# Kernel tuning notes

Hardware: AMD Instinct MI355X
Metric: run time of the kernel (lower is better)

The kernel has to match this reference:

```python
import jax, jax.numpy as jnp
import numpy as np

EPS = 1e-5


def gcn_conv(x, row, col, W, b, num_nodes):
    """PyG GCNConv: out = D^-1/2 (A+I) D^-1/2 (x W) + b, edges as (row=src, col=dst)."""
    loop = jnp.arange(num_nodes, dtype=row.dtype)
    r = jnp.concatenate([row, loop])
    c = jnp.concatenate([col, loop])
    ones = jnp.ones(c.shape[0], dtype=x.dtype)
    deg = jax.ops.segment_sum(ones, c, num_segments=num_nodes)
    dinv = jnp.where(deg > 0, jax.lax.rsqrt(deg), 0.0)
    norm = dinv[r] * dinv[c]                      # [E+N]
    xw = x @ W                                    # [N, out]
    msg = xw[r] * norm[:, None]                   # [E+N, out]
    out = jax.ops.segment_sum(msg, c, num_segments=num_nodes)
    return out + b


def layer_norm(h, g, b):
    mu = jnp.mean(h, axis=-1, keepdims=True)
    var = jnp.mean(jnp.square(h - mu), axis=-1, keepdims=True)
    return (h - mu) * jax.lax.rsqrt(var + EPS) * g + b


def setup_inputs() -> dict:
    key = jax.random.key(0)
    ks = jax.random.split(key, 12)
    B, S, D, H = 64, 512, 64, 128
    E = 524288
    A1, A2 = 5, 5
    N = B * S

    def xavier(k, shape):
        fan_in, fan_out = shape[0], shape[1]
        lim = np.sqrt(6.0 / (fan_in + fan_out))
        return jax.random.uniform(k, shape, jnp.float32, -lim, lim)

    return {
        "x": jax.random.normal(ks[0], (B, S, D), jnp.float32),
        "edge_index": jax.random.randint(ks[1], (2, E), 0, N, jnp.int64),
        "W1": xavier(ks[2], (D, H)),
        "b1": jnp.zeros((H,), jnp.float32),
        "W2": xavier(ks[3], (H, H)),
        "b2": jnp.zeros((H,), jnp.float32),
        "ln_g": jnp.ones((H,), jnp.float32),
        "ln_b": jnp.zeros((H,), jnp.float32),
        "Wq1": xavier(ks[4], (H, A1)),
        "bq1": jnp.zeros((A1,), jnp.float32),
        "Wq2": xavier(ks[5], (H, A2)),
        "bq2": jnp.zeros((A2,), jnp.float32),
    }


def reference(x, edge_index, W1, b1, W2, b2, ln_g, ln_b, Wq1, bq1, Wq2, bq2):
    B, S, D = x.shape
    N = B * S
    x_flat = x.reshape(N, D)
    row, col = edge_index[0], edge_index[1]
    # two GCN layers (dropout is identity in eval), relu activation, then LayerNorm
    h = jax.nn.relu(gcn_conv(x_flat, row, col, W1, b1, N))
    h = jax.nn.relu(gcn_conv(h, row, col, W2, b2, N))
    h = layer_norm(h, ln_g, ln_b)
    h = h.reshape(B, S, -1)
    # mode='q': per-action-dimension Q heads + hidden features
    q1 = h @ Wq1 + bq1
    q2 = h @ Wq2 + bq2
    return q1, q2, h
```

## Files before the change

kernel.cpp:

```cpp
#include <hip/hip_runtime.h>

#define HDIM 128
#define SLOT 64

typedef decltype(__builtin_amdgcn_cvt_pkrtz(0.0f, 0.0f)) h2;

__device__ __forceinline__ unsigned pack_h2(float a, float b) {
    h2 v = __builtin_amdgcn_cvt_pkrtz(a, b);
    return __builtin_bit_cast(unsigned, v);
}
__device__ __forceinline__ unsigned addh2(unsigned A, unsigned B) {
    h2 r = __builtin_bit_cast(h2, A) + __builtin_bit_cast(h2, B);
    return __builtin_bit_cast(unsigned, r);
}
__device__ __forceinline__ float2 h2f(unsigned A) {
    h2 v = __builtin_bit_cast(h2, A);
    return make_float2((float)v.x, (float)v.y);
}
__device__ __forceinline__ float dot2f(unsigned a, unsigned b, float c) {
#if __has_builtin(__builtin_amdgcn_fdot2)
    return __builtin_amdgcn_fdot2(__builtin_bit_cast(h2, a),
                                  __builtin_bit_cast(h2, b), c, false);
#else
    float2 fa = h2f(a), fb = h2f(b);
    return c + fa.x * fb.x + fa.y * fb.y;
#endif
}

__global__ void prep_kernel(int* __restrict__ cnt, int* __restrict__ xs1N,
                            int* __restrict__ xs2N, int N) {
    int i = blockIdx.x * blockDim.x + threadIdx.x;
    if (i < N) cnt[i] = 0;
    if (i < 64) { xs1N[i] = 0; xs2N[i] = 0; }
}

__global__ void fill_kernel(const int* __restrict__ row, const int* __restrict__ col,
                            int* __restrict__ cnt, ushort* __restrict__ slots, int E) {
    int i = blockIdx.x * blockDim.x + threadIdx.x;
    int e0 = 2 * i;
    if (e0 + 1 < E) {
        int2 r2 = *(const int2*)(row + e0);
        int2 c2 = *(const int2*)(col + e0);
        int p0 = atomicAdd(&cnt[c2.x], 1);
        if (p0 < SLOT - 1) slots[(long)c2.x * SLOT + p0] = (ushort)r2.x;
        int p1 = atomicAdd(&cnt[c2.y], 1);
        if (p1 < SLOT - 1) slots[(long)c2.y * SLOT + p1] = (ushort)r2.y;
    } else if (e0 < E) {
        int c = col[e0];
        int p = atomicAdd(&cnt[c], 1);
        if (p < SLOT - 1) slots[(long)c * SLOT + p] = (ushort)row[e0];
    }
}

template<int K, int NPB>
__global__ void gemm_scale_kernel(const float* __restrict__ X, const float* __restrict__ W,
                                  const int* __restrict__ cnt,
                                  unsigned* __restrict__ xs, int N) {
    __shared__ float xr[NPB * K];
    int t  = threadIdx.x;
    int n0 = blockIdx.x * NPB;
    for (int i = t; i < NPB * K; i += 128)
        xr[i] = X[(long)n0 * K + i];
    __syncthreads();

    float acc[NPB];
#pragma unroll
    for (int m = 0; m < NPB; ++m) acc[m] = 0.f;

    for (int k = 0; k < K; ++k) {
        float w = W[k * HDIM + t];
#pragma unroll
        for (int m = 0; m < NPB; ++m) acc[m] += xr[m * K + k] * w;
    }

#pragma unroll
    for (int m = 0; m < NPB; ++m) {
        int n = n0 + m;
        if (n < N) {
            float v = acc[m] * rsqrtf((float)(cnt[n] + 1));
            float w = __shfl_xor(v, 1);
            if (!(t & 1))
                xs[(long)n * 64 + (t >> 1)] = pack_h2(v, w);
        }
    }
}

__global__ __launch_bounds__(512)
void gather_gemm2_kernel(const int* __restrict__ cnt, const ushort* __restrict__ slots,
                         const unsigned* __restrict__ xs1,
                         const float* __restrict__ b1, const float* __restrict__ W2,
                         unsigned* __restrict__ xs2, int N) {
    __shared__ uint2 w2p[64 * 64];
    __shared__ unsigned hs2[8][64];
    int tid = threadIdx.x;
    for (int j = tid; j < 64 * 64; j += 512) {
        int kk = j >> 6;
        int c  = j & 63;
        const float* wr0 = W2 + (2 * kk) * HDIM;
        const float* wr1 = W2 + (2 * kk + 1) * HDIM;
        uint2 u;
        u.x = pack_h2(wr0[2 * c],     wr1[2 * c]);
        u.y = pack_h2(wr0[2 * c + 1], wr1[2 * c + 1]);
        w2p[j] = u;
    }
    __syncthreads();

    int wave = tid >> 6;
    int lane = tid & 63;
    int node = blockIdx.x * 8 + wave;
    if (node >= N) return;

    int degN = cnt[node];
    int degS = degN < (SLOT - 1) ? degN : (SLOT - 1);
    float di = rsqrtf((float)(degN + 1));

    int idx = N;
    if (lane == 0)          idx = node;
    else if (lane <= degS)  idx = (int)slots[(long)node * SLOT + lane - 1];

    unsigned accA = 0, accB = 0;
    int m = degS + 1;
    for (int k = 0; k < m; k += 8) {
        int r[8];
#pragma unroll
        for (int i = 0; i < 8; ++i) r[i] = __shfl(idx, k + i);
        unsigned u[8];
#pragma unroll
        for (int i = 0; i < 8; ++i) u[i] = xs1[((long)r[i] << 6) + lane];
#pragma unroll
        for (int i = 0; i < 8; i += 2) {
            accA = addh2(accA, u[i]);
            accB = addh2(accB, u[i + 1]);
        }
    }

    float2 t2 = h2f(addh2(accA, accB));
    int d0 = 2 * lane;
    float vx = t2.x * di + b1[d0];
    float vy = t2.y * di + b1[d0 + 1];
    vx = vx > 0.f ? vx : 0.f;
    vy = vy > 0.f ? vy : 0.f;

    hs2[wave][lane] = pack_h2(vx, vy);

    float a0 = 0.f, a1 = 0.f;
#pragma unroll 4
    for (int kk = 0; kk < 64; ++kk) {
        unsigned hb = hs2[wave][kk];
        uint2 w = w2p[kk * 64 + lane];
        a0 = dot2f(hb, w.x, a0);
        a1 = dot2f(hb, w.y, a1);
    }
    xs2[((long)node << 6) + lane] = pack_h2(a0 * di, a1 * di);
}

__global__ __launch_bounds__(512)
void gather_ln_kernel(const int* __restrict__ cnt, const ushort* __restrict__ slots,
                      const unsigned* __restrict__ xs,
                      const float* __restrict__ bvec, float* __restrict__ out,
                      const float* __restrict__ lng, const float* __restrict__ lnb,
                      const float* __restrict__ Wq1, const float* __restrict__ bq1,
                      const float* __restrict__ Wq2, const float* __restrict__ bq2,
                      float* __restrict__ q1, float* __restrict__ q2, int N) {
    __shared__ float w1s[HDIM * 5];
    __shared__ float w2s[HDIM * 5];
    for (int i = threadIdx.x; i < HDIM * 5; i += 512) {
        w1s[i] = Wq1[i];
        w2s[i] = Wq2[i];
    }
    __syncthreads();

    int wave = threadIdx.x >> 6;
    int lane = threadIdx.x & 63;
    int node = blockIdx.x * 8 + wave;
    if (node >= N) return;

    int degN = cnt[node];
    int degS = degN < (SLOT - 1) ? degN : (SLOT - 1);
    float di = rsqrtf((float)(degN + 1));

    int idx = N;
    if (lane == 0)          idx = node;
    else if (lane <= degS)  idx = (int)slots[(long)node * SLOT + lane - 1];

    unsigned accA = 0, accB = 0;
    int m = degS + 1;
    for (int k = 0; k < m; k += 8) {
        int r[8];
#pragma unroll
        for (int i = 0; i < 8; ++i) r[i] = __shfl(idx, k + i);
        unsigned u[8];
#pragma unroll
        for (int i = 0; i < 8; ++i) u[i] = xs[((long)r[i] << 6) + lane];
#pragma unroll
        for (int i = 0; i < 8; i += 2) {
            accA = addh2(accA, u[i]);
            accB = addh2(accB, u[i + 1]);
        }
    }

    float2 t2 = h2f(addh2(accA, accB));
    int d0 = 2 * lane;
    float vx = t2.x * di + bvec[d0];
    float vy = t2.y * di + bvec[d0 + 1];
    vx = vx > 0.f ? vx : 0.f;
    vy = vy > 0.f ? vy : 0.f;

    float sm = vx + vy, ss = vx * vx + vy * vy;
#pragma unroll
    for (int off = 32; off >= 1; off >>= 1) {
        sm += __shfl_xor(sm, off);
        ss += __shfl_xor(ss, off);
    }
    float mu  = sm * (1.0f / HDIM);
    float var = ss * (1.0f / HDIM) - mu * mu;
    float rs  = rsqrtf(var + 1e-5f);

    float h0 = (vx - mu) * rs * lng[d0]     + lnb[d0];
    float h1 = (vy - mu) * rs * lng[d0 + 1] + lnb[d0 + 1];
    ((float2*)(out + ((long)node << 7)))[lane] = make_float2(h0, h1);

    float p1[5], p2[5];
#pragma unroll
    for (int j = 0; j < 5; ++j) {
        p1[j] = h0 * w1s[d0 * 5 + j] + h1 * w1s[(d0 + 1) * 5 + j];
        p2[j] = h0 * w2s[d0 * 5 + j] + h1 * w2s[(d0 + 1) * 5 + j];
    }
#pragma unroll
    for (int off = 32; off >= 1; off >>= 1) {
#pragma unroll
        for (int j = 0; j < 5; ++j) {
            p1[j] += __shfl_xor(p1[j], off);
            p2[j] += __shfl_xor(p2[j], off);
        }
    }
    if (lane == 0) {
#pragma unroll
        for (int j = 0; j < 5; ++j) {
            q1[(long)node * 5 + j] = p1[j] + bq1[j];
            q2[(long)node * 5 + j] = p2[j] + bq2[j];
        }
    }
}

extern "C" void kernel_launch(void* const* d_in, const int* in_sizes, int n_in,
                              void* d_out, int out_size, void* d_ws, size_t ws_size,
                              hipStream_t stream) {
    const float* x    = (const float*)d_in[0];
    const int*   ei   = (const int*)d_in[1];
    const float* W1   = (const float*)d_in[2];
    const float* b1   = (const float*)d_in[3];
    const float* W2   = (const float*)d_in[4];
    const float* b2   = (const float*)d_in[5];
    const float* lng  = (const float*)d_in[6];
    const float* lnb  = (const float*)d_in[7];
    const float* Wq1  = (const float*)d_in[8];
    const float* bq1  = (const float*)d_in[9];
    const float* Wq2  = (const float*)d_in[10];
    const float* bq2  = (const float*)d_in[11];

    const int D = 64;
    int N = in_sizes[0] / D;
    int E = in_sizes[1] / 2;
    const int* row = ei;
    const int* col = ei + E;

    unsigned* xs1   = (unsigned*)d_ws;
    unsigned* xs2   = xs1 + (long)(N + 1) * 64;
    int*      cnt   = (int*)(xs2 + (long)(N + 1) * 64);
    ushort*   slots = (ushort*)(cnt + N);

    float* q1   = (float*)d_out;
    float* q2   = q1 + (long)N * 5;
    float* hout = q2 + (long)N * 5;

    int NB = (N + 255) / 256;

    prep_kernel<<<NB, 256, 0, stream>>>(cnt, (int*)(xs1 + (long)N * 64),
                                        (int*)(xs2 + (long)N * 64), N);
    fill_kernel<<<(E / 2 + 255) / 256, 256, 0, stream>>>(row, col, cnt, slots, E);

    gemm_scale_kernel<64, 8><<<(N + 7) / 8, 128, 0, stream>>>(x, W1, cnt, xs1, N);

    gather_gemm2_kernel<<<(N + 7) / 8, 512, 0, stream>>>(
        cnt, slots, xs1, b1, W2, xs2, N);

    gather_ln_kernel<<<(N + 7) / 8, 512, 0, stream>>>(
        cnt, slots, xs2, b2, hout,
        lng, lnb, Wq1, bq1, Wq2, bq2, q1, q2, N);
}
```

Before: 137.1 us.

## Widen edge fill to int4 with nontemporal slot stores and enlarge gemm tile

The edge-fill kernel now processes four edges per thread with int4 loads and writes slot entries with nontemporal stores, so fewer threads are launched and the scattered slot writes are meant to bypass the cache. The first GEMM kernel handles 16 nodes per block instead of 8, reusing each W1 load across more rows at the cost of more registers. Zeroing of the sentinel padding rows moves from the prep kernel into the GEMM and gather kernels. Nontemporal stores may hurt if the gather kernels later read slots from cache.

```diff
diff --git a/kernel.cpp b/kernel.cpp
--- a/kernel.cpp
+++ b/kernel.cpp
@@ -27,28 +27,33 @@
 #endif
 }
 
-__global__ void prep_kernel(int* __restrict__ cnt, int* __restrict__ xs1N,
-                            int* __restrict__ xs2N, int N) {
+__global__ void prep_kernel(int* __restrict__ cnt, int N) {
     int i = blockIdx.x * blockDim.x + threadIdx.x;
     if (i < N) cnt[i] = 0;
-    if (i < 64) { xs1N[i] = 0; xs2N[i] = 0; }
 }
 
 __global__ void fill_kernel(const int* __restrict__ row, const int* __restrict__ col,
                             int* __restrict__ cnt, ushort* __restrict__ slots, int E) {
     int i = blockIdx.x * blockDim.x + threadIdx.x;
-    int e0 = 2 * i;
-    if (e0 + 1 < E) {
-        int2 r2 = *(const int2*)(row + e0);
-        int2 c2 = *(const int2*)(col + e0);
-        int p0 = atomicAdd(&cnt[c2.x], 1);
-        if (p0 < SLOT - 1) slots[(long)c2.x * SLOT + p0] = (ushort)r2.x;
-        int p1 = atomicAdd(&cnt[c2.y], 1);
-        if (p1 < SLOT - 1) slots[(long)c2.y * SLOT + p1] = (ushort)r2.y;
-    } else if (e0 < E) {
-        int c = col[e0];
-        int p = atomicAdd(&cnt[c], 1);
-        if (p < SLOT - 1) slots[(long)c * SLOT + p] = (ushort)row[e0];
+    int e0 = 4 * i;
+    if (e0 + 3 < E) {
+        int4 r4 = *(const int4*)(row + e0);
+        int4 c4 = *(const int4*)(col + e0);
+        int p;
+        p = atomicAdd(&cnt[c4.x], 1);
+        if (p < SLOT - 1) __builtin_nontemporal_store((ushort)r4.x, &slots[(long)c4.x * SLOT + p]);
+        p = atomicAdd(&cnt[c4.y], 1);
+        if (p < SLOT - 1) __builtin_nontemporal_store((ushort)r4.y, &slots[(long)c4.y * SLOT + p]);
+        p = atomicAdd(&cnt[c4.z], 1);
+        if (p < SLOT - 1) __builtin_nontemporal_store((ushort)r4.z, &slots[(long)c4.z * SLOT + p]);
+        p = atomicAdd(&cnt[c4.w], 1);
+        if (p < SLOT - 1) __builtin_nontemporal_store((ushort)r4.w, &slots[(long)c4.w * SLOT + p]);
+    } else {
+        for (int e = e0; e < E; ++e) {
+            int c = col[e];
+            int p = atomicAdd(&cnt[c], 1);
+            if (p < SLOT - 1) __builtin_nontemporal_store((ushort)row[e], &slots[(long)c * SLOT + p]);
+        }
     }
 }
 
@@ -83,6 +88,8 @@
                 xs[(long)n * 64 + (t >> 1)] = pack_h2(v, w);
         }
     }
+
+    if (blockIdx.x == 0 && t < 64) xs[(long)N * 64 + t] = 0u;
 }
 
 __global__ __launch_bounds__(512)
@@ -103,6 +110,7 @@
         u.y = pack_h2(wr0[2 * c + 1], wr1[2 * c + 1]);
         w2p[j] = u;
     }
+    if (blockIdx.x == 0 && tid < 64) xs2[(long)N * 64 + tid] = 0u;
     __syncthreads();
 
     int wave = tid >> 6;
@@ -276,11 +284,10 @@
 
     int NB = (N + 255) / 256;
 
-    prep_kernel<<<NB, 256, 0, stream>>>(cnt, (int*)(xs1 + (long)N * 64),
-                                        (int*)(xs2 + (long)N * 64), N);
-    fill_kernel<<<(E / 2 + 255) / 256, 256, 0, stream>>>(row, col, cnt, slots, E);
-
-    gemm_scale_kernel<64, 8><<<(N + 7) / 8, 128, 0, stream>>>(x, W1, cnt, xs1, N);
+    prep_kernel<<<NB, 256, 0, stream>>>(cnt, N);
+    fill_kernel<<<(E / 4 + 255) / 256, 256, 0, stream>>>(row, col, cnt, slots, E);
+
+    gemm_scale_kernel<64, 16><<<(N + 15) / 16, 128, 0, stream>>>(x, W1, cnt, xs1, N);
 
     gather_gemm2_kernel<<<(N + 7) / 8, 512, 0, stream>>>(
         cnt, slots, xs1, b1, W2, xs2, N);
```

New measurement: 142.2 us. 1.04x slower.
